# Performance work log

Hardware: AMD Instinct MI355X
Metric: run time of the kernel (lower is better)

Reference implementation:

```python
import jax, jax.numpy as jnp
import numpy as np

B, S, TAGSET = 64, 512, 62
T = TAGSET + 2  # + START (index T-2) and END (index T-1)


def setup_inputs() -> dict:
    key = jax.random.key(0)
    k1, k2, k3, k4 = jax.random.split(key, 4)
    feats = jax.random.normal(k1, (B, S, T), dtype=jnp.float32)
    # transitions param (torch init is zeros; small random for a non-degenerate baseline)
    transitions = 0.01 * jax.random.normal(k2, (T, T), dtype=jnp.float32)
    # variable-length contiguous-prefix mask (CRF assumes mask[:, 0] == 1)
    lengths = jax.random.randint(k3, (B,), S // 2, S + 1)
    mask = (jnp.arange(S)[None, :] < lengths[:, None]).astype(jnp.int32)
    tags = jax.random.randint(k4, (B, S), 0, TAGSET).astype(jnp.int32)
    return {"feats": feats, "transitions": transitions, "mask": mask, "tags": tags}


def _nll(feats, transitions, mask, tags):
    b, s, t = feats.shape
    maskb = mask.astype(bool)
    feats_t = jnp.transpose(feats, (1, 0, 2))  # [S, B, T]
    mask_t = jnp.transpose(maskb, (1, 0))       # [S, B]

    # ---- partition function (calculate_PZ) ----
    start = t - 2
    init_part = feats_t[0] + transitions[start][None, :]  # [B, T]

    def step(part, inp):
        f_t, m_t = inp  # f_t: [B, T] emissions, m_t: [B]
        # scores[b, i, j] = part[b, i] + transitions[i, j] + f_t[b, j]
        cur = jax.nn.logsumexp(
            part[:, :, None] + transitions[None, :, :] + f_t[:, None, :], axis=1
        )  # [B, T]
        part = jnp.where(m_t[:, None], cur, part)
        return part, None

    part, _ = jax.lax.scan(step, init_part, (feats_t[1:], mask_t[1:]))
    final = jax.nn.logsumexp(part[:, :, None] + transitions[None, :, :], axis=1)
    forward_score = final[:, t - 1].sum()  # transition into END

    # ---- gold score (score_sentence) ----
    tags = tags.astype(jnp.int32)
    prev = jnp.concatenate(
        [jnp.full((b, 1), start, dtype=jnp.int32), tags[:, :-1]], axis=1
    )  # [B, S] previous tag (START at t=0)
    emit = jnp.take_along_axis(feats, tags[..., None].astype(jnp.int32), axis=2)[..., 0]
    trans = transitions[prev, tags]  # [B, S]
    tg_energy = jnp.where(maskb, emit + trans, 0.0).sum()
    lengths = mask.astype(jnp.int32).sum(axis=1)  # [B]
    end_ids = jnp.take_along_axis(tags, (lengths - 1)[:, None], axis=1)[:, 0]
    end_energy = transitions[end_ids, t - 1].sum()
    gold_score = tg_energy + end_energy

    return forward_score - gold_score


def reference(feats, transitions, mask, tags):
    return _nll(feats, transitions, mask, tags)
```

## Files before the change

kernel.cpp:

```cpp
#include <hip/hip_runtime.h>


#define SS 512
#define TT 64
#define CC 8
#define KCH 64
#define START_TAG 62
#define END_TAG 63
#define LOG2E_F 1.44269504088896340736f
#define LN2_F 0.69314718055994530942f

#define WS_ECOL_OFF 4194304
#define WS_GOLD_OFF 4325376
#define WS_EF_OFF   4325632
#define MSTR 72

typedef float v4f __attribute__((ext_vector_type(4)));
typedef _Float16 h4 __attribute__((ext_vector_type(4)));
typedef __fp16 c2 __attribute__((ext_vector_type(2)));
union H4u { h4 v; struct { c2 lo, hi; } p; };

__global__ __launch_bounds__(256, 1)
void crf_prep(const float* __restrict__ feats, const float* __restrict__ trans,
              const int* __restrict__ mask, const int* __restrict__ tags,
              float* __restrict__ out, float* __restrict__ Gg,
              _Float16* __restrict__ Ef) {
    const int c = blockIdx.x;
    const int tid = threadIdx.x;
    const int w = tid >> 6;
    __shared__ int li[4];
    __shared__ float gf[4];
    __shared__ int Lsh;

    int m = mask[c * SS + tid] + mask[c * SS + 256 + tid];
#pragma unroll
    for (int s_ = 1; s_ < 64; s_ <<= 1) m += __shfl_xor(m, s_, 64);
    if ((tid & 63) == 0) li[w] = m;
    __syncthreads();
    if (tid == 0) Lsh = li[0] + li[1] + li[2] + li[3];
    __syncthreads();
    const int Lc = Lsh;

    float g = 0.f;
#pragma unroll
    for (int rep = 0; rep < 2; ++rep) {
        int t = tid + rep * 256;
        if (t < Lc) {
            int cur = tags[c * SS + t];
            int prev = (t == 0) ? START_TAG : tags[c * SS + t - 1];
            g += feats[(size_t)c * SS * TT + (size_t)t * TT + cur] + trans[prev * TT + cur];
        }
    }
    if (tid == 0) g += trans[tags[c * SS + Lc - 1] * TT + END_TAG];
#pragma unroll
    for (int s_ = 1; s_ < 64; s_ <<= 1) g += __shfl_xor(g, s_, 64);
    if ((tid & 63) == 0) gf[w] = g;
    __syncthreads();
    if (tid == 0) Gg[c] = gf[0] + gf[1] + gf[2] + gf[3];

    if (c == 0) {
#pragma unroll
        for (int k = 0; k < 16; ++k) {
            int idx = tid + k * 256;
            Ef[idx] = (_Float16)expf(trans[idx]);
        }
        if (tid == 0) out[0] = 0.f;
    }
}

__device__ __forceinline__ void cstep(const h4 (&A)[4][4], h4 (&B)[4],
                                      float* __restrict__ emb, float& fq,
                                      const float* __restrict__ fcol, int tload,
                                      int q, int l, int& esum, int& esc) {
    v4f z = {0.f, 0.f, 0.f, 0.f};
    v4f D[4];
#pragma unroll
    for (int mt = 0; mt < 4; ++mt) {
        v4f a = __builtin_amdgcn_mfma_f32_16x16x16f16(A[mt][0], B[0], z, 0, 0, 0);
        a = __builtin_amdgcn_mfma_f32_16x16x16f16(A[mt][1], B[1], a, 0, 0, 0);
        v4f b = __builtin_amdgcn_mfma_f32_16x16x16f16(A[mt][2], B[2], z, 0, 0, 0);
        b = __builtin_amdgcn_mfma_f32_16x16x16f16(A[mt][3], B[3], b, 0, 0, 0);
        D[mt] = a + b;
    }
    v4f em[4];
#pragma unroll
    for (int mt = 0; mt < 4; ++mt) em[mt] = *(const v4f*)(emb + 16 * mt + 4 * q);
    emb[l] = __builtin_amdgcn_exp2f(fq * LOG2E_F);
    fq = fcol[(size_t)tload * TT];
    esum += esc;
    float scf = __uint_as_float((unsigned)(127 - esc) << 23);
    v4f qs[4];
#pragma unroll
    for (int mt = 0; mt < 4; ++mt) qs[mt] = D[mt] * (em[mt] * scf);
#pragma unroll
    for (int mt = 0; mt < 4; ++mt) {
        H4u u;
        u.p.lo = __builtin_amdgcn_cvt_pkrtz(qs[mt].x, qs[mt].y);
        u.p.hi = __builtin_amdgcn_cvt_pkrtz(qs[mt].z, qs[mt].w);
        B[mt] = u.v;
    }
    unsigned u0 = (unsigned)__builtin_amdgcn_readfirstlane((int)__float_as_uint(qs[0].x));
    esc = (int)((u0 >> 23) & 255u) - 127;
}

__global__ __launch_bounds__(256, 1)
void crf_chunks(const float* __restrict__ feats, const int* __restrict__ mask,
                const _Float16* __restrict__ Ef, unsigned short* __restrict__ Pg,
                int* __restrict__ Eg) {
    __shared__ float emA[4][2][TT];
    __shared__ float emB[4][2][TT];
    __shared__ __align__(16) _Float16 mld[TT * MSTR];
    __shared__ int ebuf[4];

    const int blk = blockIdx.x;
    const int chain = blk >> 3, c = blk & 7;
    const int tid = threadIdx.x;
    const int w = tid >> 6, l = tid & 63;
    const int n16 = l & 15, q = l >> 4;
    const int ncol = 16 * w + n16;

    h4 A[4][4];
#pragma unroll
    for (int mt = 0; mt < 4; ++mt)
#pragma unroll
        for (int ks = 0; ks < 4; ++ks) {
            h4 a;
#pragma unroll
            for (int e = 0; e < 4; ++e)
                a[e] = Ef[(16 * ks + 4 * q + e) * TT + 16 * mt + n16];
            A[mt][ks] = a;
        }

    const int* mp = mask + chain * SS;
    int msum = 0;
#pragma unroll
    for (int k = 0; k < 8; ++k) msum += mp[k * 64 + l];
#pragma unroll
    for (int s_ = 1; s_ < 64; s_ <<= 1) msum += __shfl_xor(msum, s_, 64);
    const int L = msum;

    const int t0a = 1 + KCH * c;
    const int t0b = t0a + 32;
    int nliveA = (L - 1) - KCH * c;
    nliveA = nliveA < 0 ? 0 : (nliveA > 32 ? 32 : nliveA);
    int nliveB = (L - 1) - KCH * c - 32;
    nliveB = nliveB < 0 ? 0 : (nliveB > 32 ? 32 : nliveB);

    h4 BA[4], BB[4];
#pragma unroll
    for (int ks = 0; ks < 4; ++ks) {
        h4 b;
#pragma unroll
        for (int j = 0; j < 4; ++j)
            b[j] = (_Float16)((16 * ks + 4 * q + j == ncol) ? 1.f : 0.f);
        BA[ks] = b;
        BB[ks] = b;
    }

    const float* fcol = feats + (size_t)chain * SS * TT + l;
#define CLAMP_T(x) ((x) < SS ? (x) : SS - 1)
    emA[w][0][l] = __builtin_amdgcn_exp2f(fcol[(size_t)CLAMP_T(t0a) * TT] * LOG2E_F);
    emA[w][1][l] = __builtin_amdgcn_exp2f(fcol[(size_t)CLAMP_T(t0a + 1) * TT] * LOG2E_F);
    emB[w][0][l] = __builtin_amdgcn_exp2f(fcol[(size_t)CLAMP_T(t0b) * TT] * LOG2E_F);
    emB[w][1][l] = __builtin_amdgcn_exp2f(fcol[(size_t)CLAMP_T(t0b + 1) * TT] * LOG2E_F);
    float fqA0 = fcol[(size_t)CLAMP_T(t0a + 2) * TT];
    float fqA1 = fcol[(size_t)CLAMP_T(t0a + 3) * TT];
    float fqB0 = fcol[(size_t)CLAMP_T(t0b + 2) * TT];
    float fqB1 = fcol[(size_t)CLAMP_T(t0b + 3) * TT];

    int esumA = 0, escA = 0, esumB = 0, escB = 0;

    const int nB2 = nliveB & ~1;
    int s = 0;
    for (; s < nB2; s += 2) {
        cstep(A, BA, &emA[w][0][0], fqA0, fcol, CLAMP_T(t0a + s + 4), q, l, esumA, escA);
        cstep(A, BB, &emB[w][0][0], fqB0, fcol, CLAMP_T(t0b + s + 4), q, l, esumB, escB);
        cstep(A, BA, &emA[w][1][0], fqA1, fcol, CLAMP_T(t0a + s + 5), q, l, esumA, escA);
        cstep(A, BB, &emB[w][1][0], fqB1, fcol, CLAMP_T(t0b + s + 5), q, l, esumB, escB);
    }
    if (nliveB & 1)
        cstep(A, BB, &emB[w][0][0], fqB0, fcol, SS - 1, q, l, esumB, escB);
    for (; s + 1 < nliveA; s += 2) {
        cstep(A, BA, &emA[w][0][0], fqA0, fcol, CLAMP_T(t0a + s + 4), q, l, esumA, escA);
        cstep(A, BA, &emA[w][1][0], fqA1, fcol, CLAMP_T(t0a + s + 5), q, l, esumA, escA);
    }
    if (s < nliveA)
        cstep(A, BA, &emA[w][0][0], fqA0, fcol, SS - 1, q, l, esumA, escA);
#undef CLAMP_T

    if (l == 0) ebuf[w] = esumB;
    __syncthreads();
    int eBmax = max(max(ebuf[0], ebuf[1]), max(ebuf[2], ebuf[3]));
    {
        _Float16 scl = (_Float16)ldexpf(1.f, esumB - eBmax);
        h4 s4 = {scl, scl, scl, scl};
#pragma unroll
        for (int ks = 0; ks < 4; ++ks) {
            h4 v = BB[ks] * s4;
#pragma unroll
            for (int j = 0; j < 4; ++j)
                mld[(16 * ks + 4 * q + j) * MSTR + ncol] = v[j];
        }
    }
    __syncthreads();
    h4 AH[4][4];
#pragma unroll
    for (int mt = 0; mt < 4; ++mt)
#pragma unroll
        for (int ks = 0; ks < 4; ++ks)
            AH[mt][ks] = *(const h4*)(mld + (16 * mt + n16) * MSTR + 16 * ks + 4 * q);
    v4f z = {0.f, 0.f, 0.f, 0.f};
    h4 Rf[4];
#pragma unroll
    for (int mt = 0; mt < 4; ++mt) {
        v4f a = __builtin_amdgcn_mfma_f32_16x16x16f16(AH[mt][0], BA[0], z, 0, 0, 0);
        a = __builtin_amdgcn_mfma_f32_16x16x16f16(AH[mt][1], BA[1], a, 0, 0, 0);
        v4f b = __builtin_amdgcn_mfma_f32_16x16x16f16(AH[mt][2], BA[2], z, 0, 0, 0);
        b = __builtin_amdgcn_mfma_f32_16x16x16f16(AH[mt][3], BA[3], b, 0, 0, 0);
        v4f d = a + b;
        H4u u;
        u.p.lo = __builtin_amdgcn_cvt_pkrtz(d.x, d.y);
        u.p.hi = __builtin_amdgcn_cvt_pkrtz(d.z, d.w);
        Rf[mt] = u.v;
    }
    __syncthreads();
#pragma unroll
    for (int mt = 0; mt < 4; ++mt)
#pragma unroll
        for (int j = 0; j < 4; ++j)
            mld[(16 * mt + 4 * q + j) * MSTR + ncol] = Rf[mt][j];
    __syncthreads();
    {
        const size_t base = ((size_t)chain * CC + c) * 4096;
        int r = tid >> 2, cb = tid & 3;
        const uint4* src = (const uint4*)(mld + r * MSTR + cb * 16);
        uint4* dst = (uint4*)(Pg + base + r * TT + cb * 16);
        dst[0] = src[0];
        dst[1] = src[1];
    }
    if (q == 0) Eg[(chain * CC + c) * TT + ncol] = esumA + eBmax;
}

__global__ __launch_bounds__(64, 1)
void crf_combine(const float* __restrict__ feats, const float* __restrict__ trans,
                 const unsigned short* __restrict__ Pg, const int* __restrict__ Eg,
                 const float* __restrict__ Gg, float* __restrict__ out) {
    __shared__ __align__(16) float yl[TT];
    const int chain = blockIdx.x;
    const int j = threadIdx.x;

    float part0 = feats[(size_t)chain * SS * TT + j] + trans[START_TAG * TT + j];
    float M0 = part0;
#pragma unroll
    for (int m = 1; m < 64; m <<= 1) M0 = fmaxf(M0, __shfl_xor(M0, m, 64));
    float x = exp2f((part0 - M0) * LOG2E_F);
    int esumX = 0;

    for (int c = 0; c < CC; ++c) {
        int e = Eg[(chain * CC + c) * TT + j];
        int emax = e;
#pragma unroll
        for (int m = 1; m < 64; m <<= 1) emax = max(emax, __shfl_xor(emax, m, 64));
        yl[j] = ldexpf(x, e - emax);
        float yv[64];
        {
            const uint4* yq = (const uint4*)yl;
#pragma unroll
            for (int i = 0; i < 16; ++i) {
                union { uint4 u; float f[4]; } cv;
                cv.u = yq[i];
                yv[4 * i + 0] = cv.f[0]; yv[4 * i + 1] = cv.f[1];
                yv[4 * i + 2] = cv.f[2]; yv[4 * i + 3] = cv.f[3];
            }
        }
        const uint4* rp = (const uint4*)(Pg + ((size_t)chain * CC + c) * 4096 + (size_t)j * TT);
        float acc = 0.f;
#pragma unroll
        for (int i = 0; i < 8; ++i) {
            union { uint4 u; _Float16 h[8]; } pv;
            pv.u = rp[i];
#pragma unroll
            for (int k2 = 0; k2 < 8; ++k2)
                acc = __builtin_fmaf((float)pv.h[k2], yv[8 * i + k2], acc);
        }
        float am = acc;
#pragma unroll
        for (int m = 1; m < 64; m <<= 1) am = fmaxf(am, __shfl_xor(am, m, 64));
        int e0 = (int)((__float_as_uint(am) >> 23) & 255u) - 127;
        x = ldexpf(acc, -e0);
        esumX += e0 + emax;
    }

    float val = x * expf(trans[j * TT + END_TAG]);
#pragma unroll
    for (int m = 1; m < 64; m <<= 1) val += __shfl_xor(val, m, 64);
    float fwd = logf(val) + (float)esumX * LN2_F + M0;
    if (j == 0) atomicAdd(out, fwd);

    if (chain == 0) {
        float gv = Gg[j];
#pragma unroll
        for (int m = 1; m < 64; m <<= 1) gv += __shfl_xor(gv, m, 64);
        if (j == 0) atomicAdd(out, -gv);
    }
}

extern "C" void kernel_launch(void* const* d_in, const int* in_sizes, int n_in,
                              void* d_out, int out_size, void* d_ws, size_t ws_size,
                              hipStream_t stream) {
    const float* feats = (const float*)d_in[0];
    const float* trans = (const float*)d_in[1];
    const int*   mask  = (const int*)d_in[2];
    const int*   tags  = (const int*)d_in[3];
    float* out = (float*)d_out;
    unsigned short* Pg = (unsigned short*)d_ws;
    int*       Eg = (int*)((char*)d_ws + WS_ECOL_OFF);
    float*     Gg = (float*)((char*)d_ws + WS_GOLD_OFF);
    _Float16*  Ef = (_Float16*)((char*)d_ws + WS_EF_OFF);

    crf_prep<<<dim3(64), dim3(256), 0, stream>>>(feats, trans, mask, tags, out, Gg, Ef);
    crf_chunks<<<dim3(64 * CC), dim3(256), 0, stream>>>(feats, mask, Ef, Pg, Eg);
    crf_combine<<<dim3(64), dim3(64), 0, stream>>>(feats, trans, Pg, Eg, Gg, out);
}
```

Baseline: 111.9 us.

## Split chunks into four interleaved sub-chains and drop the prep kernel

Each block now runs four independent 16-step sub-chains at once instead of two 32-step ones, which shortens the serial MFMA dependency chain and adds more instruction-level parallelism. The partial transfer matrices are then merged with extra matrix products through shared memory. The prep kernel is removed. exp(transitions) is computed inline in each chunk block, the gold score moves into the combine kernel, and the output is zeroed by block 0. This saves one kernel launch but adds more merge MFMAs, register pressure and a possible race on the output zeroing.

```diff
diff --git a/kernel.cpp b/kernel.cpp
--- a/kernel.cpp
+++ b/kernel.cpp
@@ -11,62 +11,12 @@
 #define LN2_F 0.69314718055994530942f
 
 #define WS_ECOL_OFF 4194304
-#define WS_GOLD_OFF 4325376
-#define WS_EF_OFF   4325632
 #define MSTR 72
 
 typedef float v4f __attribute__((ext_vector_type(4)));
 typedef _Float16 h4 __attribute__((ext_vector_type(4)));
 typedef __fp16 c2 __attribute__((ext_vector_type(2)));
 union H4u { h4 v; struct { c2 lo, hi; } p; };
-
-__global__ __launch_bounds__(256, 1)
-void crf_prep(const float* __restrict__ feats, const float* __restrict__ trans,
-              const int* __restrict__ mask, const int* __restrict__ tags,
-              float* __restrict__ out, float* __restrict__ Gg,
-              _Float16* __restrict__ Ef) {
-    const int c = blockIdx.x;
-    const int tid = threadIdx.x;
-    const int w = tid >> 6;
-    __shared__ int li[4];
-    __shared__ float gf[4];
-    __shared__ int Lsh;
-
-    int m = mask[c * SS + tid] + mask[c * SS + 256 + tid];
-#pragma unroll
-    for (int s_ = 1; s_ < 64; s_ <<= 1) m += __shfl_xor(m, s_, 64);
-    if ((tid & 63) == 0) li[w] = m;
-    __syncthreads();
-    if (tid == 0) Lsh = li[0] + li[1] + li[2] + li[3];
-    __syncthreads();
-    const int Lc = Lsh;
-
-    float g = 0.f;
-#pragma unroll
-    for (int rep = 0; rep < 2; ++rep) {
-        int t = tid + rep * 256;
-        if (t < Lc) {
-            int cur = tags[c * SS + t];
-            int prev = (t == 0) ? START_TAG : tags[c * SS + t - 1];
-            g += feats[(size_t)c * SS * TT + (size_t)t * TT + cur] + trans[prev * TT + cur];
-        }
-    }
-    if (tid == 0) g += trans[tags[c * SS + Lc - 1] * TT + END_TAG];
-#pragma unroll
-    for (int s_ = 1; s_ < 64; s_ <<= 1) g += __shfl_xor(g, s_, 64);
-    if ((tid & 63) == 0) gf[w] = g;
-    __syncthreads();
-    if (tid == 0) Gg[c] = gf[0] + gf[1] + gf[2] + gf[3];
-
-    if (c == 0) {
-#pragma unroll
-        for (int k = 0; k < 16; ++k) {
-            int idx = tid + k * 256;
-            Ef[idx] = (_Float16)expf(trans[idx]);
-        }
-        if (tid == 0) out[0] = 0.f;
-    }
-}
 
 __device__ __forceinline__ void cstep(const h4 (&A)[4][4], h4 (&B)[4],
                                       float* __restrict__ emb, float& fq,
@@ -104,13 +54,13 @@
 }
 
 __global__ __launch_bounds__(256, 1)
-void crf_chunks(const float* __restrict__ feats, const int* __restrict__ mask,
-                const _Float16* __restrict__ Ef, unsigned short* __restrict__ Pg,
-                int* __restrict__ Eg) {
-    __shared__ float emA[4][2][TT];
-    __shared__ float emB[4][2][TT];
-    __shared__ __align__(16) _Float16 mld[TT * MSTR];
-    __shared__ int ebuf[4];
+void crf_chunks(const float* __restrict__ feats, const float* __restrict__ trans,
+                const int* __restrict__ mask, unsigned short* __restrict__ Pg,
+                int* __restrict__ Eg, float* __restrict__ out) {
+    __shared__ float em[4][4][2][TT];
+    __shared__ __align__(16) _Float16 mldB[TT * MSTR];
+    __shared__ __align__(16) _Float16 mldD[TT * MSTR];
+    __shared__ int ebuf[12];
 
     const int blk = blockIdx.x;
     const int chain = blk >> 3, c = blk & 7;
@@ -119,6 +69,8 @@
     const int n16 = l & 15, q = l >> 4;
     const int ncol = 16 * w + n16;
 
+    if (blk == 0 && tid == 0) out[0] = 0.f;
+
     h4 A[4][4];
 #pragma unroll
     for (int mt = 0; mt < 4; ++mt)
@@ -127,7 +79,8 @@
             h4 a;
 #pragma unroll
             for (int e = 0; e < 4; ++e)
-                a[e] = Ef[(16 * ks + 4 * q + e) * TT + 16 * mt + n16];
+                a[e] = (_Float16)__builtin_amdgcn_exp2f(
+                    trans[(16 * ks + 4 * q + e) * TT + 16 * mt + n16] * LOG2E_F);
             A[mt][ks] = a;
         }
 
@@ -140,114 +93,229 @@
     const int L = msum;
 
     const int t0a = 1 + KCH * c;
-    const int t0b = t0a + 32;
-    int nliveA = (L - 1) - KCH * c;
-    nliveA = nliveA < 0 ? 0 : (nliveA > 32 ? 32 : nliveA);
-    int nliveB = (L - 1) - KCH * c - 32;
-    nliveB = nliveB < 0 ? 0 : (nliveB > 32 ? 32 : nliveB);
-
-    h4 BA[4], BB[4];
+    const int t0b = t0a + 16, t0c = t0a + 32, t0d = t0a + 48;
+    const int base = (L - 1) - KCH * c;
+    int nA = base < 0 ? 0 : (base > 16 ? 16 : base);
+    int nB = base - 16 < 0 ? 0 : (base - 16 > 16 ? 16 : base - 16);
+    int nC = base - 32 < 0 ? 0 : (base - 32 > 16 ? 16 : base - 32);
+    int nD = base - 48 < 0 ? 0 : (base - 48 > 16 ? 16 : base - 48);
+
+    h4 Ba[4], Bb[4], Bc[4], Bd[4];
 #pragma unroll
     for (int ks = 0; ks < 4; ++ks) {
         h4 b;
 #pragma unroll
-        for (int j = 0; j < 4; ++j)
-            b[j] = (_Float16)((16 * ks + 4 * q + j == ncol) ? 1.f : 0.f);
-        BA[ks] = b;
-        BB[ks] = b;
+        for (int jj = 0; jj < 4; ++jj)
+            b[jj] = (_Float16)((16 * ks + 4 * q + jj == ncol) ? 1.f : 0.f);
+        Ba[ks] = b; Bb[ks] = b; Bc[ks] = b; Bd[ks] = b;
     }
 
     const float* fcol = feats + (size_t)chain * SS * TT + l;
-#define CLAMP_T(x) ((x) < SS ? (x) : SS - 1)
-    emA[w][0][l] = __builtin_amdgcn_exp2f(fcol[(size_t)CLAMP_T(t0a) * TT] * LOG2E_F);
-    emA[w][1][l] = __builtin_amdgcn_exp2f(fcol[(size_t)CLAMP_T(t0a + 1) * TT] * LOG2E_F);
-    emB[w][0][l] = __builtin_amdgcn_exp2f(fcol[(size_t)CLAMP_T(t0b) * TT] * LOG2E_F);
-    emB[w][1][l] = __builtin_amdgcn_exp2f(fcol[(size_t)CLAMP_T(t0b + 1) * TT] * LOG2E_F);
-    float fqA0 = fcol[(size_t)CLAMP_T(t0a + 2) * TT];
-    float fqA1 = fcol[(size_t)CLAMP_T(t0a + 3) * TT];
-    float fqB0 = fcol[(size_t)CLAMP_T(t0b + 2) * TT];
-    float fqB1 = fcol[(size_t)CLAMP_T(t0b + 3) * TT];
-
-    int esumA = 0, escA = 0, esumB = 0, escB = 0;
-
-    const int nB2 = nliveB & ~1;
-    int s = 0;
-    for (; s < nB2; s += 2) {
-        cstep(A, BA, &emA[w][0][0], fqA0, fcol, CLAMP_T(t0a + s + 4), q, l, esumA, escA);
-        cstep(A, BB, &emB[w][0][0], fqB0, fcol, CLAMP_T(t0b + s + 4), q, l, esumB, escB);
-        cstep(A, BA, &emA[w][1][0], fqA1, fcol, CLAMP_T(t0a + s + 5), q, l, esumA, escA);
-        cstep(A, BB, &emB[w][1][0], fqB1, fcol, CLAMP_T(t0b + s + 5), q, l, esumB, escB);
-    }
-    if (nliveB & 1)
-        cstep(A, BB, &emB[w][0][0], fqB0, fcol, SS - 1, q, l, esumB, escB);
-    for (; s + 1 < nliveA; s += 2) {
-        cstep(A, BA, &emA[w][0][0], fqA0, fcol, CLAMP_T(t0a + s + 4), q, l, esumA, escA);
-        cstep(A, BA, &emA[w][1][0], fqA1, fcol, CLAMP_T(t0a + s + 5), q, l, esumA, escA);
-    }
-    if (s < nliveA)
-        cstep(A, BA, &emA[w][0][0], fqA0, fcol, SS - 1, q, l, esumA, escA);
-#undef CLAMP_T
-
-    if (l == 0) ebuf[w] = esumB;
-    __syncthreads();
-    int eBmax = max(max(ebuf[0], ebuf[1]), max(ebuf[2], ebuf[3]));
+#define CT(x) ((x) < SS ? (x) : SS - 1)
+    em[0][w][0][l] = __builtin_amdgcn_exp2f(fcol[(size_t)CT(t0a) * TT] * LOG2E_F);
+    em[0][w][1][l] = __builtin_amdgcn_exp2f(fcol[(size_t)CT(t0a + 1) * TT] * LOG2E_F);
+    em[1][w][0][l] = __builtin_amdgcn_exp2f(fcol[(size_t)CT(t0b) * TT] * LOG2E_F);
+    em[1][w][1][l] = __builtin_amdgcn_exp2f(fcol[(size_t)CT(t0b + 1) * TT] * LOG2E_F);
+    em[2][w][0][l] = __builtin_amdgcn_exp2f(fcol[(size_t)CT(t0c) * TT] * LOG2E_F);
+    em[2][w][1][l] = __builtin_amdgcn_exp2f(fcol[(size_t)CT(t0c + 1) * TT] * LOG2E_F);
+    em[3][w][0][l] = __builtin_amdgcn_exp2f(fcol[(size_t)CT(t0d) * TT] * LOG2E_F);
+    em[3][w][1][l] = __builtin_amdgcn_exp2f(fcol[(size_t)CT(t0d + 1) * TT] * LOG2E_F);
+    float fqA0 = fcol[(size_t)CT(t0a + 2) * TT];
+    float fqA1 = fcol[(size_t)CT(t0a + 3) * TT];
+    float fqB0 = fcol[(size_t)CT(t0b + 2) * TT];
+    float fqB1 = fcol[(size_t)CT(t0b + 3) * TT];
+    float fqC0 = fcol[(size_t)CT(t0c + 2) * TT];
+    float fqC1 = fcol[(size_t)CT(t0c + 3) * TT];
+    float fqD0 = fcol[(size_t)CT(t0d + 2) * TT];
+    float fqD1 = fcol[(size_t)CT(t0d + 3) * TT];
+
+    int esA = 0, escA = 0, esB = 0, escB = 0;
+    int esC = 0, escC = 0, esD = 0, escD = 0;
+
+    if (nD == 16) {
+        for (int r = 0; r < 8; ++r) {
+            const int s0 = 2 * r;
+            cstep(A, Ba, &em[0][w][0][0], fqA0, fcol, CT(t0a + s0 + 4), q, l, esA, escA);
+            cstep(A, Bb, &em[1][w][0][0], fqB0, fcol, CT(t0b + s0 + 4), q, l, esB, escB);
+            cstep(A, Bc, &em[2][w][0][0], fqC0, fcol, CT(t0c + s0 + 4), q, l, esC, escC);
+            cstep(A, Bd, &em[3][w][0][0], fqD0, fcol, CT(t0d + s0 + 4), q, l, esD, escD);
+            cstep(A, Ba, &em[0][w][1][0], fqA1, fcol, CT(t0a + s0 + 5), q, l, esA, escA);
+            cstep(A, Bb, &em[1][w][1][0], fqB1, fcol, CT(t0b + s0 + 5), q, l, esB, escB);
+            cstep(A, Bc, &em[2][w][1][0], fqC1, fcol, CT(t0c + s0 + 5), q, l, esC, escC);
+            cstep(A, Bd, &em[3][w][1][0], fqD1, fcol, CT(t0d + s0 + 5), q, l, esD, escD);
+        }
+    } else {
+        for (int r = 0; r < 8; ++r) {
+            const int s0 = 2 * r, s1 = s0 + 1;
+            if (s0 < nA) cstep(A, Ba, &em[0][w][0][0], fqA0, fcol, CT(t0a + s0 + 4), q, l, esA, escA);
+            if (s0 < nB) cstep(A, Bb, &em[1][w][0][0], fqB0, fcol, CT(t0b + s0 + 4), q, l, esB, escB);
+            if (s0 < nC) cstep(A, Bc, &em[2][w][0][0], fqC0, fcol, CT(t0c + s0 + 4), q, l, esC, escC);
+            if (s0 < nD) cstep(A, Bd, &em[3][w][0][0], fqD0, fcol, CT(t0d + s0 + 4), q, l, esD, escD);
+            if (s1 < nA) cstep(A, Ba, &em[0][w][1][0], fqA1, fcol, CT(t0a + s1 + 4), q, l, esA, escA);
+            if (s1 < nB) cstep(A, Bb, &em[1][w][1][0], fqB1, fcol, CT(t0b + s1 + 4), q, l, esB, escB);
+            if (s1 < nC) cstep(A, Bc, &em[2][w][1][0], fqC1, fcol, CT(t0c + s1 + 4), q, l, esC, escC);
+            if (s1 < nD) cstep(A, Bd, &em[3][w][1][0], fqD1, fcol, CT(t0d + s1 + 4), q, l, esD, escD);
+        }
+    }
+#undef CT
+
+    if (l == 0) { ebuf[w] = esB; ebuf[4 + w] = esD; }
+    __syncthreads();
+    const int eBmax = max(max(ebuf[0], ebuf[1]), max(ebuf[2], ebuf[3]));
+    const int eDmax = max(max(ebuf[4], ebuf[5]), max(ebuf[6], ebuf[7]));
     {
-        _Float16 scl = (_Float16)ldexpf(1.f, esumB - eBmax);
-        h4 s4 = {scl, scl, scl, scl};
+        _Float16 sB = (_Float16)ldexpf(1.f, esB - eBmax);
+        _Float16 sD = (_Float16)ldexpf(1.f, esD - eDmax);
+        h4 s4B = {sB, sB, sB, sB}, s4D = {sD, sD, sD, sD};
 #pragma unroll
         for (int ks = 0; ks < 4; ++ks) {
-            h4 v = BB[ks] * s4;
-#pragma unroll
-            for (int j = 0; j < 4; ++j)
-                mld[(16 * ks + 4 * q + j) * MSTR + ncol] = v[j];
-        }
-    }
-    __syncthreads();
-    h4 AH[4][4];
+            h4 vb = Bb[ks] * s4B;
+            h4 vd = Bd[ks] * s4D;
+#pragma unroll
+            for (int jj = 0; jj < 4; ++jj) {
+                mldB[(16 * ks + 4 * q + jj) * MSTR + ncol] = vb[jj];
+                mldD[(16 * ks + 4 * q + jj) * MSTR + ncol] = vd[jj];
+            }
+        }
+    }
+    __syncthreads();
+    h4 AHb[4][4], AHd[4][4];
 #pragma unroll
     for (int mt = 0; mt < 4; ++mt)
 #pragma unroll
+        for (int ks = 0; ks < 4; ++ks) {
+            AHb[mt][ks] = *(const h4*)(mldB + (16 * mt + n16) * MSTR + 16 * ks + 4 * q);
+            AHd[mt][ks] = *(const h4*)(mldD + (16 * mt + n16) * MSTR + 16 * ks + 4 * q);
+        }
+    v4f z = {0.f, 0.f, 0.f, 0.f};
+    v4f P1[4], P2[4];
+#pragma unroll
+    for (int mt = 0; mt < 4; ++mt) {
+        v4f a = __builtin_amdgcn_mfma_f32_16x16x16f16(AHb[mt][0], Ba[0], z, 0, 0, 0);
+        a = __builtin_amdgcn_mfma_f32_16x16x16f16(AHb[mt][1], Ba[1], a, 0, 0, 0);
+        v4f b = __builtin_amdgcn_mfma_f32_16x16x16f16(AHb[mt][2], Ba[2], z, 0, 0, 0);
+        b = __builtin_amdgcn_mfma_f32_16x16x16f16(AHb[mt][3], Ba[3], b, 0, 0, 0);
+        P1[mt] = a + b;
+        v4f a2 = __builtin_amdgcn_mfma_f32_16x16x16f16(AHd[mt][0], Bc[0], z, 0, 0, 0);
+        a2 = __builtin_amdgcn_mfma_f32_16x16x16f16(AHd[mt][1], Bc[1], a2, 0, 0, 0);
+        v4f b2 = __builtin_amdgcn_mfma_f32_16x16x16f16(AHd[mt][2], Bc[2], z, 0, 0, 0);
+        b2 = __builtin_amdgcn_mfma_f32_16x16x16f16(AHd[mt][3], Bc[3], b2, 0, 0, 0);
+        P2[mt] = a2 + b2;
+    }
+    float m1 = 0.f, m2 = 0.f;
+#pragma unroll
+    for (int mt = 0; mt < 4; ++mt) {
+        m1 = fmaxf(m1, fmaxf(fmaxf(P1[mt].x, P1[mt].y), fmaxf(P1[mt].z, P1[mt].w)));
+        m2 = fmaxf(m2, fmaxf(fmaxf(P2[mt].x, P2[mt].y), fmaxf(P2[mt].z, P2[mt].w)));
+    }
+#pragma unroll
+    for (int m = 1; m < 64; m <<= 1) {
+        m1 = fmaxf(m1, __shfl_xor(m1, m, 64));
+        m2 = fmaxf(m2, __shfl_xor(m2, m, 64));
+    }
+    unsigned u1 = (unsigned)__builtin_amdgcn_readfirstlane((int)__float_as_uint(m1));
+    unsigned u2 = (unsigned)__builtin_amdgcn_readfirstlane((int)__float_as_uint(m2));
+    const int e1c = u1 ? (int)((u1 >> 23) & 255u) - 127 : 0;
+    const int e2c = u2 ? (int)((u2 >> 23) & 255u) - 127 : 0;
+    const int e1 = esA + eBmax + e1c;
+    const int e2 = esC + eDmax + e2c;
+    h4 P1h[4], P2h[4];
+    {
+        float s1f = __uint_as_float((unsigned)(127 - e1c) << 23);
+        float s2f = __uint_as_float((unsigned)(127 - e2c) << 23);
+#pragma unroll
+        for (int mt = 0; mt < 4; ++mt) {
+            v4f q1 = P1[mt] * s1f;
+            v4f q2 = P2[mt] * s2f;
+            H4u ua, ub;
+            ua.p.lo = __builtin_amdgcn_cvt_pkrtz(q1.x, q1.y);
+            ua.p.hi = __builtin_amdgcn_cvt_pkrtz(q1.z, q1.w);
+            ub.p.lo = __builtin_amdgcn_cvt_pkrtz(q2.x, q2.y);
+            ub.p.hi = __builtin_amdgcn_cvt_pkrtz(q2.z, q2.w);
+            P1h[mt] = ua.v;
+            P2h[mt] = ub.v;
+        }
+    }
+
+    if (l == 0) ebuf[8 + w] = e2;
+    __syncthreads();
+    const int e2max = max(max(ebuf[8], ebuf[9]), max(ebuf[10], ebuf[11]));
+    {
+        _Float16 s2 = (_Float16)ldexpf(1.f, e2 - e2max);
+        h4 s4 = {s2, s2, s2, s2};
+#pragma unroll
+        for (int mt = 0; mt < 4; ++mt) {
+            h4 v = P2h[mt] * s4;
+#pragma unroll
+            for (int jj = 0; jj < 4; ++jj)
+                mldB[(16 * mt + 4 * q + jj) * MSTR + ncol] = v[jj];
+        }
+    }
+    __syncthreads();
+    h4 AHp[4][4];
+#pragma unroll
+    for (int mt = 0; mt < 4; ++mt)
+#pragma unroll
         for (int ks = 0; ks < 4; ++ks)
-            AH[mt][ks] = *(const h4*)(mld + (16 * mt + n16) * MSTR + 16 * ks + 4 * q);
-    v4f z = {0.f, 0.f, 0.f, 0.f};
+            AHp[mt][ks] = *(const h4*)(mldB + (16 * mt + n16) * MSTR + 16 * ks + 4 * q);
     h4 Rf[4];
 #pragma unroll
     for (int mt = 0; mt < 4; ++mt) {
-        v4f a = __builtin_amdgcn_mfma_f32_16x16x16f16(AH[mt][0], BA[0], z, 0, 0, 0);
-        a = __builtin_amdgcn_mfma_f32_16x16x16f16(AH[mt][1], BA[1], a, 0, 0, 0);
-        v4f b = __builtin_amdgcn_mfma_f32_16x16x16f16(AH[mt][2], BA[2], z, 0, 0, 0);
-        b = __builtin_amdgcn_mfma_f32_16x16x16f16(AH[mt][3], BA[3], b, 0, 0, 0);
+        v4f a = __builtin_amdgcn_mfma_f32_16x16x16f16(AHp[mt][0], P1h[0], z, 0, 0, 0);
+        a = __builtin_amdgcn_mfma_f32_16x16x16f16(AHp[mt][1], P1h[1], a, 0, 0, 0);
+        v4f b = __builtin_amdgcn_mfma_f32_16x16x16f16(AHp[mt][2], P1h[2], z, 0, 0, 0);
+        b = __builtin_amdgcn_mfma_f32_16x16x16f16(AHp[mt][3], P1h[3], b, 0, 0, 0);
         v4f d = a + b;
         H4u u;
         u.p.lo = __builtin_amdgcn_cvt_pkrtz(d.x, d.y);
         u.p.hi = __builtin_amdgcn_cvt_pkrtz(d.z, d.w);
         Rf[mt] = u.v;
     }
-    __syncthreads();
 #pragma unroll
     for (int mt = 0; mt < 4; ++mt)
 #pragma unroll
-        for (int j = 0; j < 4; ++j)
-            mld[(16 * mt + 4 * q + j) * MSTR + ncol] = Rf[mt][j];
+        for (int jj = 0; jj < 4; ++jj)
+            mldD[(16 * mt + 4 * q + jj) * MSTR + ncol] = Rf[mt][jj];
     __syncthreads();
     {
-        const size_t base = ((size_t)chain * CC + c) * 4096;
+        const size_t base_ = ((size_t)chain * CC + c) * 4096;
         int r = tid >> 2, cb = tid & 3;
-        const uint4* src = (const uint4*)(mld + r * MSTR + cb * 16);
-        uint4* dst = (uint4*)(Pg + base + r * TT + cb * 16);
+        const uint4* src = (const uint4*)(mldD + r * MSTR + cb * 16);
+        uint4* dst = (uint4*)(Pg + base_ + r * TT + cb * 16);
         dst[0] = src[0];
         dst[1] = src[1];
     }
-    if (q == 0) Eg[(chain * CC + c) * TT + ncol] = esumA + eBmax;
+    if (q == 0) Eg[(chain * CC + c) * TT + ncol] = e1 + e2max;
 }
 
 __global__ __launch_bounds__(64, 1)
 void crf_combine(const float* __restrict__ feats, const float* __restrict__ trans,
+                 const int* __restrict__ mask, const int* __restrict__ tags,
                  const unsigned short* __restrict__ Pg, const int* __restrict__ Eg,
-                 const float* __restrict__ Gg, float* __restrict__ out) {
+                 float* __restrict__ out) {
     __shared__ __align__(16) float yl[TT];
     const int chain = blockIdx.x;
     const int j = threadIdx.x;
+
+    int msum = 0;
+#pragma unroll
+    for (int k = 0; k < 8; ++k) msum += mask[chain * SS + 64 * k + j];
+#pragma unroll
+    for (int m = 1; m < 64; m <<= 1) msum += __shfl_xor(msum, m, 64);
+    const int L = msum;
+
+    float g = 0.f;
+#pragma unroll
+    for (int k = 0; k < 8; ++k) {
+        int t = 64 * k + j;
+        if (t < L) {
+            int cur = tags[chain * SS + t];
+            int prev = t ? tags[chain * SS + t - 1] : START_TAG;
+            g += feats[(size_t)chain * SS * TT + (size_t)t * TT + cur] + trans[prev * TT + cur];
+        }
+    }
+#pragma unroll
+    for (int m = 1; m < 64; m <<= 1) g += __shfl_xor(g, m, 64);
 
     float part0 = feats[(size_t)chain * SS * TT + j] + trans[START_TAG * TT + j];
     float M0 = part0;
@@ -295,13 +363,10 @@
 #pragma unroll
     for (int m = 1; m < 64; m <<= 1) val += __shfl_xor(val, m, 64);
     float fwd = logf(val) + (float)esumX * LN2_F + M0;
-    if (j == 0) atomicAdd(out, fwd);
-
-    if (chain == 0) {
-        float gv = Gg[j];
-#pragma unroll
-        for (int m = 1; m < 64; m <<= 1) gv += __shfl_xor(gv, m, 64);
-        if (j == 0) atomicAdd(out, -gv);
+
+    if (j == 0) {
+        float gold = g + trans[tags[chain * SS + L - 1] * TT + END_TAG];
+        atomicAdd(out, fwd - gold);
     }
 }
 
@@ -315,10 +380,7 @@
     float* out = (float*)d_out;
     unsigned short* Pg = (unsigned short*)d_ws;
     int*       Eg = (int*)((char*)d_ws + WS_ECOL_OFF);
-    float*     Gg = (float*)((char*)d_ws + WS_GOLD_OFF);
-    _Float16*  Ef = (_Float16*)((char*)d_ws + WS_EF_OFF);
-
-    crf_prep<<<dim3(64), dim3(256), 0, stream>>>(feats, trans, mask, tags, out, Gg, Ef);
-    crf_chunks<<<dim3(64 * CC), dim3(256), 0, stream>>>(feats, mask, Ef, Pg, Eg);
-    crf_combine<<<dim3(64), dim3(64), 0, stream>>>(feats, trans, Pg, Eg, Gg, out);
+
+    crf_chunks<<<dim3(64 * CC), dim3(256), 0, stream>>>(feats, trans, mask, Pg, Eg, out);
+    crf_combine<<<dim3(64), dim3(64), 0, stream>>>(feats, trans, mask, tags, Pg, Eg, out);
 }
```

Result: no change. 113.5 us (+1.4%).
